# Kernel optimization log

Measured on AMD Instinct MI355X. Metric: run time of the kernel, lower is better.

Reference implementation:

```python
import jax, jax.numpy as jnp
import numpy as np

S = 1024   # speakers_per_batch
U = 64     # utterances_per_speaker
D = 256    # embedding_size
EPS = 1e-5


def setup_inputs() -> dict:
    key = jax.random.key(0)
    k1, = jax.random.split(key, 1)
    return {
        "output_of_model": jax.random.normal(k1, (S * U, D), dtype=jnp.float32),
        "similarity_weight": jnp.array([10.0], dtype=jnp.float32),
        "similarity_bias": jnp.array([-5.0], dtype=jnp.float32),
        "speakers_per_batch": S,
        "utterances_per_speaker": U,
    }


def reference(output_of_model, similarity_weight, similarity_bias,
              speakers_per_batch, utterances_per_speaker):
    s, u = speakers_per_batch, utterances_per_speaker
    embeds = output_of_model.reshape(s, u, -1)                      # [S,U,D]

    # inclusive centroids (mean over utterances, L2-normalized with +eps)
    c_incl = jnp.mean(embeds, axis=1)                               # [S,D]
    c_incl = c_incl / (jnp.linalg.norm(c_incl, axis=-1, keepdims=True) + EPS)

    # exclusive centroids (leave-one-out mean, L2-normalized with +eps)
    c_excl = (jnp.sum(embeds, axis=1, keepdims=True) - embeds) / (u - 1)  # [S,U,D]
    c_excl = c_excl / (jnp.linalg.norm(c_excl, axis=-1, keepdims=True) + EPS)

    # normalized embeddings (original normalizes embeds inside the loop)
    e_n = embeds / (jnp.linalg.norm(embeds, axis=-1, keepdims=True) + EPS)

    # off-diagonal: cosine(embed[i,u], incl centroid[j]); diagonal: excl centroid
    sim_incl = jnp.einsum('sud,jd->suj', e_n, c_incl)               # [S,U,S]
    sim_excl = jnp.sum(e_n * c_excl, axis=-1)                       # [S,U]
    diag = jnp.eye(s, dtype=bool)[:, None, :]                       # [S,1,S]
    sim = jnp.where(diag, sim_excl[:, :, None], sim_incl)           # [S,U,S]

    sim = sim * similarity_weight + similarity_bias                 # scaled logits

    logits = sim.reshape(s * u, s)
    targets = jnp.repeat(jnp.arange(s), u)                          # ground truth
    logp = jax.nn.log_softmax(logits, axis=-1)
    loss = -jnp.mean(jnp.take_along_axis(logp, targets[:, None], axis=-1))
    return loss
```

## Files before the change

### kernel.cpp

```cpp
#include <hip/hip_runtime.h>

#define SPK 1024
#define UTT 64
#define DIM 256
#define EPSV 1e-5f
#define NROW (SPK * UTT)
#define LOG2E 1.44269504f

typedef __attribute__((ext_vector_type(4))) float f32x4;
typedef __attribute__((ext_vector_type(2))) long long2v;

#define EXP2(x) __builtin_amdgcn_exp2f(x)

__device__ __forceinline__ int pk_fp8(float a, float b, float c, float d) {
    int v = __builtin_amdgcn_cvt_pk_fp8_f32(a, b, 0, false);
    return  __builtin_amdgcn_cvt_pk_fp8_f32(c, d, v, true);
}

__device__ __forceinline__ int fragIdx(int g) {
    return ((g >> 4) * 4 + ((g & 7) >> 1)) * 4 + ((g >> 3) & 1) * 2 + (g & 1);
}

__global__ __launch_bounds__(256)
void k_cent(const float* __restrict__ x, unsigned char* __restrict__ cincl8,
            float* __restrict__ csum, float* __restrict__ nrm) {
    __shared__ float4 sc4[256];
    int s = blockIdx.x, tid = threadIdx.x;
    int dq = tid & 63, ug = tid >> 6;
    const float4* x4 = (const float4*)(x + (size_t)s * UTT * DIM);
    float4 p = {0.f, 0.f, 0.f, 0.f};
#pragma unroll
    for (int i = 0; i < 16; ++i) {
        float4 v = x4[(ug * 16 + i) * 64 + dq];
        p.x += v.x; p.y += v.y; p.z += v.z; p.w += v.w;
    }
    sc4[tid] = p;
    __syncthreads();
    if (tid < 64) {
        float4 a = sc4[dq], b2 = sc4[64 + dq], c = sc4[128 + dq], d = sc4[192 + dq];
        float4 cs = {a.x + b2.x + c.x + d.x, a.y + b2.y + c.y + d.y,
                     a.z + b2.z + c.z + d.z, a.w + b2.w + c.w + d.w};
        ((float4*)csum)[s * 64 + dq] = cs;
        float s2 = cs.x * cs.x + cs.y * cs.y + cs.z * cs.z + cs.w * cs.w;
#pragma unroll
        for (int o = 1; o < 64; o <<= 1) s2 += __shfl_xor(s2, o);
        float inv = 16.f / (sqrtf(s2) + UTT * EPSV);
        ((int*)cincl8)[s * 64 + fragIdx(dq)] =
            pk_fp8(cs.x * inv, cs.y * inv, cs.z * inv, cs.w * inv);
        if (tid == 0) nrm[s] = s2;
    }
}

__global__ __launch_bounds__(256, 2)
void k_fused(const float* __restrict__ x, const unsigned char* __restrict__ cincl8,
             const float* __restrict__ csum, const float* __restrict__ nrm,
             const float* __restrict__ wp, const float* __restrict__ bp,
             float* __restrict__ out) {
    __shared__ unsigned char Bs[2][16 * 1024];
    __shared__ float texs[64];
    __shared__ float red[4];
    int tid = threadIdx.x, wave = tid >> 6, lane = tid & 63;
    int quad = lane >> 4, lx = lane & 15;
    int s = blockIdx.x;
    float w = wp[0], b = bp[0];
    float M  = fabsf(w) * 1.0625f + b;
    float wl = w * (LOG2E / 256.f);
    float bl = (b - M) * LOG2E;

#define STAGE(buf, t)                                                           \
    _Pragma("unroll")                                                           \
    for (int r = 0; r < 4; ++r) {                                               \
        const unsigned char* g = cincl8 +                                       \
            (size_t)((t) * 64 + wave * 16 + lx) * DIM + (r * 4 + quad) * 16;    \
        __builtin_amdgcn_global_load_lds(                                       \
            (const __attribute__((address_space(1))) void*)g,                   \
            (__attribute__((address_space(3))) void*)(Bs[buf] + (wave * 4 + r) * 1024), \
            16, 0, 0);                                                          \
    }
    STAGE(0, 0);

    int arow = wave * 16 + lx;
    const float* xr = x + ((size_t)s * UTT + arow) * DIM + quad * 8;
    const float* cb = csum + (size_t)s * DIM + quad * 8;
    float4 xv[16];
    float sx = 0.f, sc = 0.f;
#pragma unroll
    for (int kt = 0; kt < 8; ++kt) {
        float4 a0 = *(const float4*)(xr + kt * 32);
        float4 a1 = *(const float4*)(xr + kt * 32 + 4);
        float4 c0 = *(const float4*)(cb + kt * 32);
        float4 c1 = *(const float4*)(cb + kt * 32 + 4);
        xv[2 * kt] = a0; xv[2 * kt + 1] = a1;
        sx += a0.x * a0.x + a0.y * a0.y + a0.z * a0.z + a0.w * a0.w
            + a1.x * a1.x + a1.y * a1.y + a1.z * a1.z + a1.w * a1.w;
        sc += a0.x * c0.x + a0.y * c0.y + a0.z * c0.z + a0.w * c0.w
            + a1.x * c1.x + a1.y * c1.y + a1.z * c1.z + a1.w * c1.w;
    }
    sx += __shfl_xor(sx, 16); sx += __shfl_xor(sx, 32);
    sc += __shfl_xor(sc, 16); sc += __shfl_xor(sc, 32);
    float nx = sqrtf(sx);
    float inv = 16.f / (nx + EPSV);
    long af[8];
#pragma unroll
    for (int kt = 0; kt < 8; ++kt) {
        int lo = pk_fp8(xv[2 * kt].x * inv,     xv[2 * kt].y * inv,
                        xv[2 * kt].z * inv,     xv[2 * kt].w * inv);
        int hi = pk_fp8(xv[2 * kt + 1].x * inv, xv[2 * kt + 1].y * inv,
                        xv[2 * kt + 1].z * inv, xv[2 * kt + 1].w * inv);
        af[kt] = (long)(((unsigned long long)(unsigned)hi << 32) | (unsigned)lo);
    }
    if (quad == 0) {
        float scc = nrm[s];
        float num = sc - sx;
        float e2 = fmaxf(scc - 2.f * sc + sx, 0.f);
        float sim = num / ((nx + EPSV) * (sqrtf(e2) + (UTT - 1) * EPSV));
        texs[arow] = fmaf(sim, w, b);
    }

    float l[4] = {0.f, 0.f, 0.f, 0.f};
    int s_hi = s >> 6, nt_d = (s >> 4) & 3, lx_d = s & 15;
    __syncthreads();

    for (int t = 0; t < 16; ++t) {
        const unsigned char* bsc = Bs[t & 1];
        if (t < 15) { STAGE((t & 1) ^ 1, t + 1); }
#pragma unroll
        for (int nt = 0; nt < 4; ++nt) {
            long2v bf2[4];
#pragma unroll
            for (int r = 0; r < 4; ++r)
                bf2[r] = *(const long2v*)(bsc + (nt * 4 + r) * 1024 + lane * 16);
            f32x4 acc = {0.f, 0.f, 0.f, 0.f};
#pragma unroll
            for (int r = 0; r < 4; ++r) {
                acc = __builtin_amdgcn_mfma_f32_16x16x32_fp8_fp8(af[2 * r],     bf2[r].x, acc, 0, 0, 0);
                acc = __builtin_amdgcn_mfma_f32_16x16x32_fp8_fp8(af[2 * r + 1], bf2[r].y, acc, 0, 0, 0);
            }
            bool dg = (t == s_hi) && (nt == nt_d);
#pragma unroll
            for (int i = 0; i < 4; ++i) {
                float e = EXP2(fmaf(acc[i], wl, bl));
                if (!(dg && lx == lx_d)) l[i] += e;
            }
        }
        __syncthreads();
    }

#pragma unroll
    for (int o = 1; o < 16; o <<= 1)
#pragma unroll
        for (int i = 0; i < 4; ++i) l[i] += __shfl_xor(l[i], o);

    float cc = 0.f;
    if (lx == 0) {
#pragma unroll
        for (int i = 0; i < 4; ++i) {
            float tex = texs[wave * 16 + quad * 4 + i];
            cc += (M + __logf(l[i] + EXP2((tex - M) * LOG2E))) - tex;
        }
    }
#pragma unroll
    for (int o = 1; o < 64; o <<= 1) cc += __shfl_xor(cc, o);
    if (lane == 0) red[wave] = cc;
    __syncthreads();
    if (tid == 0)
        atomicAdd(out, (red[0] + red[1] + red[2] + red[3]) * (1.f / NROW));
}

extern "C" void kernel_launch(void* const* d_in, const int* in_sizes, int n_in,
                              void* d_out, int out_size, void* d_ws, size_t ws_size,
                              hipStream_t stream) {
    const float* x  = (const float*)d_in[0];
    const float* wp = (const float*)d_in[1];
    const float* bp = (const float*)d_in[2];
    char* ws = (char*)d_ws;
    unsigned char* cincl8 = (unsigned char*)ws;
    float* csum           = (float*)(ws + (1u << 19));
    float* nrm            = (float*)(ws + (2u << 20));
    float* out = (float*)d_out;

    hipMemsetAsync(d_out, 0, sizeof(float), stream);
    k_cent <<<SPK, 256, 0, stream>>>(x, cincl8, csum, nrm);
    k_fused<<<SPK, 256, 0, stream>>>(x, cincl8, csum, nrm, wp, bp, out);
}
```

Before: 144.9 us.

## Share A tile across waves, load B directly to registers, split columns per wave

Restructures the fused GEMM so each wave now holds all 64 rows of fp8 A fragments, staged once through padded shared memory. Each wave covers a distinct 16-column slice of centroids per step and reads it straight from global memory into registers with a one-step prefetch, which removes the LDS double buffer and the per-iteration barrier. Diagonal exclusion is done by subtracting the matching exp term after the fact. Per-wave partial row sums are combined through shared memory at the end. Occupancy target rises to 4 blocks per CU, at the cost of more registers for A fragments and accumulators and more global/L2 traffic for B.

```diff
diff --git a/kernel.cpp b/kernel.cpp
--- a/kernel.cpp
+++ b/kernel.cpp
@@ -6,6 +6,7 @@
 #define EPSV 1e-5f
 #define NROW (SPK * UTT)
 #define LOG2E 1.44269504f
+#define ASTRIDE 34
 
 typedef __attribute__((ext_vector_type(4))) float f32x4;
 typedef __attribute__((ext_vector_type(2))) long long2v;
@@ -51,14 +52,14 @@
     }
 }
 
-__global__ __launch_bounds__(256, 2)
+__global__ __launch_bounds__(256, 4)
 void k_fused(const float* __restrict__ x, const unsigned char* __restrict__ cincl8,
              const float* __restrict__ csum, const float* __restrict__ nrm,
              const float* __restrict__ wp, const float* __restrict__ bp,
              float* __restrict__ out) {
-    __shared__ unsigned char Bs[2][16 * 1024];
+    __shared__ long shareA[64 * ASTRIDE];
     __shared__ float texs[64];
-    __shared__ float red[4];
+    __shared__ float fin[4][64];
     int tid = threadIdx.x, wave = tid >> 6, lane = tid & 63;
     int quad = lane >> 4, lx = lane & 15;
     int s = blockIdx.x;
@@ -66,18 +67,6 @@
     float M  = fabsf(w) * 1.0625f + b;
     float wl = w * (LOG2E / 256.f);
     float bl = (b - M) * LOG2E;
-
-#define STAGE(buf, t)                                                           \
-    _Pragma("unroll")                                                           \
-    for (int r = 0; r < 4; ++r) {                                               \
-        const unsigned char* g = cincl8 +                                       \
-            (size_t)((t) * 64 + wave * 16 + lx) * DIM + (r * 4 + quad) * 16;    \
-        __builtin_amdgcn_global_load_lds(                                       \
-            (const __attribute__((address_space(1))) void*)g,                   \
-            (__attribute__((address_space(3))) void*)(Bs[buf] + (wave * 4 + r) * 1024), \
-            16, 0, 0);                                                          \
-    }
-    STAGE(0, 0);
 
     int arow = wave * 16 + lx;
     const float* xr = x + ((size_t)s * UTT + arow) * DIM + quad * 8;
@@ -100,14 +89,21 @@
     sc += __shfl_xor(sc, 16); sc += __shfl_xor(sc, 32);
     float nx = sqrtf(sx);
     float inv = 16.f / (nx + EPSV);
-    long af[8];
-#pragma unroll
-    for (int kt = 0; kt < 8; ++kt) {
-        int lo = pk_fp8(xv[2 * kt].x * inv,     xv[2 * kt].y * inv,
-                        xv[2 * kt].z * inv,     xv[2 * kt].w * inv);
-        int hi = pk_fp8(xv[2 * kt + 1].x * inv, xv[2 * kt + 1].y * inv,
-                        xv[2 * kt + 1].z * inv, xv[2 * kt + 1].w * inv);
-        af[kt] = (long)(((unsigned long long)(unsigned)hi << 32) | (unsigned)lo);
+    long* shp = &shareA[arow * ASTRIDE + quad * 8];
+#pragma unroll
+    for (int r = 0; r < 4; ++r) {
+        int a_lo = pk_fp8(xv[4 * r + 0].x * inv, xv[4 * r + 0].y * inv,
+                          xv[4 * r + 0].z * inv, xv[4 * r + 0].w * inv);
+        int a_hi = pk_fp8(xv[4 * r + 1].x * inv, xv[4 * r + 1].y * inv,
+                          xv[4 * r + 1].z * inv, xv[4 * r + 1].w * inv);
+        int b_lo = pk_fp8(xv[4 * r + 2].x * inv, xv[4 * r + 2].y * inv,
+                          xv[4 * r + 2].z * inv, xv[4 * r + 2].w * inv);
+        int b_hi = pk_fp8(xv[4 * r + 3].x * inv, xv[4 * r + 3].y * inv,
+                          xv[4 * r + 3].z * inv, xv[4 * r + 3].w * inv);
+        long2v pr;
+        pr.x = (long)(((unsigned long long)(unsigned)a_hi << 32) | (unsigned)a_lo);
+        pr.y = (long)(((unsigned long long)(unsigned)b_hi << 32) | (unsigned)b_lo);
+        *(long2v*)(shp + 2 * r) = pr;
     }
     if (quad == 0) {
         float scc = nrm[s];
@@ -116,55 +112,79 @@
         float sim = num / ((nx + EPSV) * (sqrtf(e2) + (UTT - 1) * EPSV));
         texs[arow] = fmaf(sim, w, b);
     }
-
-    float l[4] = {0.f, 0.f, 0.f, 0.f};
-    int s_hi = s >> 6, nt_d = (s >> 4) & 3, lx_d = s & 15;
     __syncthreads();
 
+    long2v af[4][4];
+#pragma unroll
+    for (int mt = 0; mt < 4; ++mt)
+#pragma unroll
+        for (int r = 0; r < 4; ++r)
+            af[mt][r] = *(const long2v*)(&shareA[(mt * 16 + lx) * ASTRIDE + quad * 8 + 2 * r]);
+
+    float l[16];
+#pragma unroll
+    for (int i = 0; i < 16; ++i) l[i] = 0.f;
+    int t_d = s >> 6, w_d = (s >> 4) & 3, lx_d = s & 15;
+    const unsigned char* bp_ = cincl8 + (size_t)(wave * 16 + lx) * DIM + quad * 16;
+
+    long2v bfc[4], bfn[4];
+#pragma unroll
+    for (int r = 0; r < 4; ++r) bfc[r] = *(const long2v*)(bp_ + r * 64);
+
     for (int t = 0; t < 16; ++t) {
-        const unsigned char* bsc = Bs[t & 1];
-        if (t < 15) { STAGE((t & 1) ^ 1, t + 1); }
-#pragma unroll
-        for (int nt = 0; nt < 4; ++nt) {
-            long2v bf2[4];
-#pragma unroll
-            for (int r = 0; r < 4; ++r)
-                bf2[r] = *(const long2v*)(bsc + (nt * 4 + r) * 1024 + lane * 16);
-            f32x4 acc = {0.f, 0.f, 0.f, 0.f};
-#pragma unroll
-            for (int r = 0; r < 4; ++r) {
-                acc = __builtin_amdgcn_mfma_f32_16x16x32_fp8_fp8(af[2 * r],     bf2[r].x, acc, 0, 0, 0);
-                acc = __builtin_amdgcn_mfma_f32_16x16x32_fp8_fp8(af[2 * r + 1], bf2[r].y, acc, 0, 0, 0);
-            }
-            bool dg = (t == s_hi) && (nt == nt_d);
-#pragma unroll
-            for (int i = 0; i < 4; ++i) {
-                float e = EXP2(fmaf(acc[i], wl, bl));
-                if (!(dg && lx == lx_d)) l[i] += e;
-            }
+        const unsigned char* bn = bp_ + (size_t)(((t + 1) & 15) * 64) * DIM;
+#pragma unroll
+        for (int r = 0; r < 4; ++r)
+            bfn[r] = *(const long2v*)(bn + r * 64);
+        f32x4 acc[4] = {{0.f,0.f,0.f,0.f},{0.f,0.f,0.f,0.f},
+                        {0.f,0.f,0.f,0.f},{0.f,0.f,0.f,0.f}};
+#pragma unroll
+        for (int r = 0; r < 4; ++r) {
+#pragma unroll
+            for (int mt = 0; mt < 4; ++mt)
+                acc[mt] = __builtin_amdgcn_mfma_f32_16x16x32_fp8_fp8(af[mt][r].x, bfc[r].x, acc[mt], 0, 0, 0);
+#pragma unroll
+            for (int mt = 0; mt < 4; ++mt)
+                acc[mt] = __builtin_amdgcn_mfma_f32_16x16x32_fp8_fp8(af[mt][r].y, bfc[r].y, acc[mt], 0, 0, 0);
         }
-        __syncthreads();
+#pragma unroll
+        for (int mt = 0; mt < 4; ++mt)
+#pragma unroll
+            for (int i = 0; i < 4; ++i)
+                l[mt * 4 + i] += EXP2(fmaf(acc[mt][i], wl, bl));
+        if (t == t_d && wave == w_d) {
+#pragma unroll
+            for (int mt = 0; mt < 4; ++mt)
+#pragma unroll
+                for (int i = 0; i < 4; ++i) {
+                    float e = EXP2(fmaf(acc[mt][i], wl, bl));
+                    if (lx == lx_d) l[mt * 4 + i] -= e;
+                }
+        }
+#pragma unroll
+        for (int r = 0; r < 4; ++r) bfc[r] = bfn[r];
     }
 
 #pragma unroll
     for (int o = 1; o < 16; o <<= 1)
 #pragma unroll
-        for (int i = 0; i < 4; ++i) l[i] += __shfl_xor(l[i], o);
-
-    float cc = 0.f;
-    if (lx == 0) {
-#pragma unroll
-        for (int i = 0; i < 4; ++i) {
-            float tex = texs[wave * 16 + quad * 4 + i];
-            cc += (M + __logf(l[i] + EXP2((tex - M) * LOG2E))) - tex;
-        }
-    }
-#pragma unroll
-    for (int o = 1; o < 64; o <<= 1) cc += __shfl_xor(cc, o);
-    if (lane == 0) red[wave] = cc;
+        for (int i = 0; i < 16; ++i) l[i] += __shfl_xor(l[i], o);
+    if (lx == 0)
+#pragma unroll
+        for (int mt = 0; mt < 4; ++mt)
+#pragma unroll
+            for (int i = 0; i < 4; ++i)
+                fin[wave][mt * 16 + quad * 4 + i] = l[mt * 4 + i];
     __syncthreads();
-    if (tid == 0)
-        atomicAdd(out, (red[0] + red[1] + red[2] + red[3]) * (1.f / NROW));
+
+    if (tid < 64) {
+        float D = fin[0][tid] + fin[1][tid] + fin[2][tid] + fin[3][tid];
+        float tex = texs[tid];
+        float cc = (M + __logf(D + EXP2((tex - M) * LOG2E))) - tex;
+#pragma unroll
+        for (int o = 1; o < 64; o <<= 1) cc += __shfl_xor(cc, o);
+        if (tid == 0) atomicAdd(out, cc * (1.f / NROW));
+    }
 }
 
 extern "C" void kernel_launch(void* const* d_in, const int* in_sizes, int n_in,
```

After: 142.0 us. -2.0%, faster.
